# Kernel tuning notes

Measured on AMD Instinct MI355X. Metric: run time of the kernel, lower is better.

## Reference

```python
import jax, jax.numpy as jnp
import numpy as np

B, K, D = 4, 2048, 512   # batch, time window (self._K), d_model
H, Q, V = 8, 64, 64      # heads, per-head query dim, per-head value dim


def setup_inputs() -> dict:
    key = jax.random.key(0)
    ks = jax.random.split(key, 10)
    s = 0.05
    return {
        "query": jax.random.normal(ks[0], (B, K, D), jnp.float32),
        "key":   jax.random.normal(ks[1], (B, K, D), jnp.float32),
        "value": jax.random.normal(ks[2], (B, K, D), jnp.float32),
        # stacked per-head Linear params (torch Linear: y = x W^T + b -> store as [h, D, out])
        "W_q": jax.random.normal(ks[3], (H, D, Q), jnp.float32) * s,
        "b_q": jax.random.normal(ks[4], (H, Q), jnp.float32) * s,
        "W_k": jax.random.normal(ks[5], (H, D, Q), jnp.float32) * s,
        "b_k": jax.random.normal(ks[6], (H, Q), jnp.float32) * s,
        "W_v": jax.random.normal(ks[7], (H, D, V), jnp.float32) * s,
        "b_v": jax.random.normal(ks[8], (H, V), jnp.float32) * s,
        "W_o": jax.random.normal(ks[9], (H * V, D), jnp.float32) * s,
        "b_o": jnp.zeros((D,), jnp.float32),
    }


def reference(query, key, value, W_q, b_q, W_k, b_k, W_v, b_v, W_o, b_o):
    # per-head projections, batched over heads: [B, H, K, Q/V]
    q = jnp.einsum("bkd,hdq->bhkq", query, W_q) + b_q[None, :, None, :]
    k = jnp.einsum("bkd,hdq->bhkq", key,   W_k) + b_k[None, :, None, :]
    v = jnp.einsum("bkd,hdv->bhkv", value, W_v) + b_v[None, :, None, :]
    # NOTE: original divides by sqrt(self._K) (time window), NOT sqrt(d_k)
    scores = jnp.einsum("bhkq,bhlq->bhkl", q, k) / np.sqrt(K).astype(np.float32)
    # mask == 'subsequent': causal triu mask above the diagonal
    causal = jnp.triu(jnp.ones((K, K), bool), k=1)
    scores = jnp.where(causal[None, None], -jnp.inf, scores)
    attn = jax.nn.softmax(scores, axis=-1)
    heads = jnp.einsum("bhkl,bhlv->bhkv", attn, v)          # [B, H, K, V]
    concat = heads.transpose(0, 2, 1, 3).reshape(B, K, H * V)  # concat along last dim
    return concat @ W_o + b_o
```

## Files before the change

### kernel.cpp

```cpp
#include <hip/hip_runtime.h>
#include <hip/hip_bf16.h>

typedef __attribute__((ext_vector_type(8))) short bf16x8;
typedef __attribute__((ext_vector_type(4))) float f32x4;

#define SEQ 2048
#define DM  512
#define NH  8
#define DH  64
#define QSCALE 0.031879360f

__device__ __forceinline__ unsigned short f2bf(float f) {
  unsigned int u = __float_as_uint(f);
  unsigned int r = 0x7FFFu + ((u >> 16) & 1u);
  return (unsigned short)((u + r) >> 16);
}

__device__ __forceinline__ void cvt8f(const float4& v0, const float4& v1,
                                      unsigned short* __restrict__ o) {
  o[0] = f2bf(v0.x); o[1] = f2bf(v0.y); o[2] = f2bf(v0.z); o[3] = f2bf(v0.w);
  o[4] = f2bf(v1.x); o[5] = f2bf(v1.y); o[6] = f2bf(v1.z); o[7] = f2bf(v1.w);
}

__device__ __forceinline__ void load8f(const float* __restrict__ s,
                                       unsigned short* __restrict__ o) {
  float4 v0 = *(const float4*)s;
  float4 v1 = *(const float4*)(s + 4);
  cvt8f(v0, v1, o);
}

__global__ __launch_bounds__(256) void weight_prep(const float* __restrict__ Wq,
                                                   const float* __restrict__ Wk,
                                                   const float* __restrict__ Wv,
                                                   const float* __restrict__ Wo,
                                                   const float* __restrict__ q,
                                                   const float* __restrict__ k,
                                                   const float* __restrict__ v,
                                                   unsigned short* __restrict__ Wqt,
                                                   unsigned short* __restrict__ Wkt,
                                                   unsigned short* __restrict__ Wvt,
                                                   unsigned short* __restrict__ Wot,
                                                   unsigned short* __restrict__ Xb) {
  const int tid = threadIdx.x;
  if (blockIdx.x >= 256) {
    const int wi = blockIdx.x - 256;
    const float* src = (wi < 128) ? q : (wi < 256) ? k : v;
    const size_t off = (size_t)(wi & 127) * 32768;
    const float* s = src + off;
    unsigned short* d = Xb + (size_t)(wi >> 7) * (4u * SEQ * DM) + off;
#pragma unroll
    for (int i = 0; i < 16; ++i) {
      const size_t idx = (size_t)(tid + 256 * i) * 8;
      __align__(16) unsigned short t[8];
      load8f(s + idx, t);
      *(uint4*)(d + idx) = *(const uint4*)t;
    }
    return;
  }
  const int which = blockIdx.x >> 6, wi = blockIdx.x & 63;
  const float* src;
  unsigned short* dst;
  int R, C, r0, c0;
  if (which < 3) {
    const float* W = (which == 0) ? Wq : (which == 1) ? Wk : Wv;
    unsigned short* D = (which == 0) ? Wqt : (which == 1) ? Wkt : Wvt;
    int h = wi >> 3;
    src = W + (size_t)h * 512 * 64;
    dst = D + (size_t)h * 64 * 512;
    R = 512; C = 64; r0 = (wi & 7) * 64; c0 = 0;
  } else {
    src = Wo; dst = Wot;
    R = 512; C = 512; r0 = (wi >> 3) * 64; c0 = (wi & 7) * 64;
  }
  __shared__ __align__(16) unsigned short T[64][72];
#pragma unroll
  for (int i = 0; i < 2; ++i) {
    int c = tid + 256 * i;
    int lr = c >> 3, lc = (c & 7) * 8;
    __align__(16) unsigned short tmp[8];
    load8f(src + (size_t)(r0 + lr) * C + c0 + lc, tmp);
    *(uint4*)&T[lr][lc] = *(const uint4*)tmp;
  }
  __syncthreads();
#pragma unroll
  for (int i = 0; i < 2; ++i) {
    int c = tid + 256 * i;
    int orow = c >> 3, och = (c & 7) * 8;
    __align__(16) unsigned short tmp[8];
#pragma unroll
    for (int j = 0; j < 8; ++j) tmp[j] = T[och + j][orow];
    *(uint4*)(dst + (size_t)(c0 + orow) * R + r0 + och) = *(uint4*)tmp;
  }
}

__global__ __launch_bounds__(256, 4) void proj128(const unsigned short* __restrict__ Xb,
                                                  const unsigned short* __restrict__ Wqt,
                                                  const unsigned short* __restrict__ Wkt,
                                                  const unsigned short* __restrict__ Wvt,
                                                  const float* __restrict__ bq,
                                                  const float* __restrict__ bk,
                                                  const float* __restrict__ bv,
                                                  unsigned short* __restrict__ Qp,
                                                  unsigned short* __restrict__ Kp,
                                                  unsigned short* __restrict__ Vpt) {
  const int which = blockIdx.z;
  const unsigned short* X = Xb + (size_t)which * (4u * SEQ * DM);
  const unsigned short* Wt = (which == 0) ? Wqt : (which == 1) ? Wkt : Wvt;
  const float* bias = (which == 0) ? bq : (which == 1) ? bk : bv;
  unsigned short* out = (which == 0) ? Qp : (which == 1) ? Kp : Vpt;
  const float ps = (which == 0) ? QSCALE : 1.0f;

  const int m0 = blockIdx.x * 128;
  const int n0 = blockIdx.y * 128;
  __shared__ __align__(16) unsigned short smem[2][128][72];
  unsigned short (*As)[72] = smem[0];
  unsigned short (*Bs)[72] = smem[1];
  const int tid  = threadIdx.x;
  const int wave = tid >> 6, lane = tid & 63;
  const int l15  = lane & 15, quad = lane >> 4;
  const int rb = (wave >> 1) * 64, cb = (wave & 1) * 64;

  f32x4 acc[4][4];
#pragma unroll
  for (int i = 0; i < 4; ++i)
#pragma unroll
    for (int f = 0; f < 4; ++f) acc[i][f] = (f32x4){0.f, 0.f, 0.f, 0.f};

  for (int k0 = 0; k0 < DM; k0 += 64) {
    __syncthreads();
#pragma unroll
    for (int i = 0; i < 4; ++i) {
      int c = tid + 256 * i;
      int lr = c >> 3, lc = (c & 7) * 8;
      *(uint4*)&As[lr][lc] = *(const uint4*)(X  + (size_t)(m0 + lr) * DM + k0 + lc);
      *(uint4*)&Bs[lr][lc] = *(const uint4*)(Wt + (size_t)(n0 + lr) * DM + k0 + lc);
    }
    __syncthreads();
#pragma unroll
    for (int kc = 0; kc < 2; ++kc) {
      bf16x8 av[4], bv4[4];
#pragma unroll
      for (int i = 0; i < 4; ++i) av[i]  = *(const bf16x8*)&As[rb + 16 * i + l15][kc * 32 + quad * 8];
#pragma unroll
      for (int f = 0; f < 4; ++f) bv4[f] = *(const bf16x8*)&Bs[cb + 16 * f + l15][kc * 32 + quad * 8];
#pragma unroll
      for (int i = 0; i < 4; ++i)
#pragma unroll
        for (int f = 0; f < 4; ++f)
          acc[i][f] = __builtin_amdgcn_mfma_f32_16x16x32_bf16(av[i], bv4[f], acc[i][f], 0, 0, 0);
    }
  }

  if (which < 2) {
#pragma unroll
    for (int i = 0; i < 4; ++i)
#pragma unroll
      for (int f = 0; f < 4; ++f)
#pragma unroll
        for (int r = 0; r < 4; ++r) {
          int m = m0 + rb + 16 * i + quad * 4 + r;
          int col = n0 + cb + 16 * f + l15;
          int head = col >> 6, o = col & 63;
          int b = m >> 11, s = m & (SEQ - 1);
          float val = (acc[i][f][r] + bias[col]) * ps;
          out[(((size_t)(b * NH + head) * SEQ + s) << 6) + o] = f2bf(val);
        }
  } else {
    __syncthreads();
    unsigned short* T = &smem[0][0][0] + wave * 4608;
#pragma unroll
    for (int i = 0; i < 4; ++i)
#pragma unroll
      for (int f = 0; f < 4; ++f)
#pragma unroll
        for (int r = 0; r < 4; ++r) {
          int lrow = 16 * i + quad * 4 + r;
          int lcol = 16 * f + l15;
          int col = n0 + cb + 16 * f + l15;
          T[lcol * 72 + lrow] = f2bf(acc[i][f][r] + bias[col]);
        }
    const int mbase = m0 + rb;
    const int b = mbase >> 11, sbase = mbase & (SEQ - 1);
    const int head = (n0 + cb) >> 6;
    unsigned short* dstb = out + ((size_t)(b * NH + head) * DH) * SEQ + sbase;
#pragma unroll
    for (int j = 0; j < 8; ++j) {
      int dh = (lane >> 3) + j * 8;
      int sc = (lane & 7) * 8;
      *(uint4*)(dstb + (size_t)dh * SEQ + sc) = *(const uint4*)&T[dh * 72 + sc];
    }
  }
}

__global__ __launch_bounds__(512, 4) void attn_kernel(const unsigned short* __restrict__ Qp,
                                                      const unsigned short* __restrict__ Kp,
                                                      const unsigned short* __restrict__ Vpt,
                                                      unsigned short* __restrict__ concat) {
  const int bh = blockIdx.x;
  const int ip = blockIdx.y;
  const int b = bh >> 3, h = bh & 7;
  const int qa = ip, qb = 31 - ip;
  __shared__ __align__(16) unsigned short Ks[2][64][72], Vts[2][64][72], Ps[128][76];
  const int tid  = threadIdx.x;
  const int wave = tid >> 6, lane = tid & 63;
  const int l15  = lane & 15, quad = lane >> 4;
  const int w4   = wave & 3;
  const bool isB = wave < 4;
  const int qt   = isB ? qb : qa;
  const unsigned short* Qb = Qp  + (size_t)bh * SEQ * DH;
  const unsigned short* Kb = Kp  + (size_t)bh * SEQ * DH;
  const unsigned short* Vb = Vpt + (size_t)bh * DH * SEQ;

  bf16x8 aq[2];
#pragma unroll
  for (int kc = 0; kc < 2; ++kc)
    aq[kc] = *(const bf16x8*)(Qb + (size_t)(qt * 64 + 16 * w4 + l15) * DH + kc * 32 + quad * 8);

  float l_lane[4];
  f32x4 Of[4];
#pragma unroll
  for (int r = 0; r < 4; ++r) l_lane[r] = 0.f;
#pragma unroll
  for (int f = 0; f < 4; ++f) Of[f] = (f32x4){0.f, 0.f, 0.f, 0.f};

  const int sr = tid >> 3, sc = (tid & 7) * 8;
  uint4 kst, vst;

#define STAGE_LOAD(lt_) do {                                                   \
    kst = *(const uint4*)(Kb + (size_t)((lt_) * 64 + sr) * DH + sc);           \
    vst = *(const uint4*)(Vb + (size_t)sr * SEQ + (lt_) * 64 + sc);            \
  } while (0)

#define STAGE_WRITE(bi_) do {                                                  \
    *(uint4*)&Ks[bi_][sr][sc]  = kst;                                          \
    *(uint4*)&Vts[bi_][sr][sc] = vst;                                          \
  } while (0)

  STAGE_LOAD(0);
  STAGE_WRITE(0);
  STAGE_LOAD(1);
  __syncthreads();

#pragma unroll 1
  for (int lt = 0; lt <= qb; ++lt) {
    const int cur = lt & 1;
    if (lt < qb) STAGE_WRITE(cur ^ 1);
    if (lt + 2 <= qb) STAGE_LOAD(lt + 2);

    const bool act = isB || (lt <= qa);
    if (act) {
      const int l0 = lt * 64;
      f32x4 S[4];
#pragma unroll
      for (int f = 0; f < 4; ++f) S[f] = (f32x4){0.f, 0.f, 0.f, 0.f};
#pragma unroll
      for (int kc = 0; kc < 2; ++kc) {
#pragma unroll
        for (int f = 0; f < 4; ++f) {
          bf16x8 bk = *(const bf16x8*)&Ks[cur][16 * f + l15][kc * 32 + quad * 8];
          S[f] = __builtin_amdgcn_mfma_f32_16x16x32_bf16(aq[kc], bk, S[f], 0, 0, 0);
        }
      }
      if (lt == qt) {
        const int mrow = qt * 64 + 16 * w4 + quad * 4;
#pragma unroll
        for (int f = 0; f < 4; ++f)
#pragma unroll
          for (int r = 0; r < 4; ++r)
            if (l0 + 16 * f + l15 > mrow + r) S[f][r] = -1e30f;
      }
#pragma unroll
      for (int f = 0; f < 4; ++f)
#pragma unroll
        for (int r = 0; r < 4; ++r) {
          float p = __builtin_amdgcn_exp2f(S[f][r]);
          l_lane[r] += p;
          Ps[wave * 16 + quad * 4 + r][16 * f + l15] = f2bf(p);
        }
#pragma unroll
      for (int kc = 0; kc < 2; ++kc) {
        bf16x8 ap = *(const bf16x8*)&Ps[wave * 16 + l15][kc * 32 + quad * 8];
#pragma unroll
        for (int f = 0; f < 4; ++f) {
          bf16x8 bvv = *(const bf16x8*)&Vts[cur][16 * f + l15][kc * 32 + quad * 8];
          Of[f] = __builtin_amdgcn_mfma_f32_16x16x32_bf16(ap, bvv, Of[f], 0, 0, 0);
        }
      }
    }
    __syncthreads();
  }
#undef STAGE_LOAD
#undef STAGE_WRITE

#pragma unroll
  for (int d = 1; d < 16; d <<= 1)
#pragma unroll
    for (int r = 0; r < 4; ++r) l_lane[r] += __shfl_xor(l_lane[r], d);

#pragma unroll
  for (int f = 0; f < 4; ++f)
#pragma unroll
    for (int r = 0; r < 4; ++r) {
      const int row = qt * 64 + 16 * w4 + quad * 4 + r;
      const int col = h * DH + 16 * f + l15;
      concat[(size_t)(b * SEQ + row) * DM + col] = f2bf(Of[f][r] / l_lane[r]);
    }
}

__global__ __launch_bounds__(256, 2) void gemm_out(const unsigned short* __restrict__ A,
                                                   const unsigned short* __restrict__ Bt,
                                                   const float* __restrict__ bias,
                                                   float* __restrict__ out) {
  const int m0 = blockIdx.x * 64;
  const int nbase = blockIdx.y * 128;
  __shared__ __align__(16) unsigned short Bs[2][64][72];
  const int tid  = threadIdx.x;
  const int wave = tid >> 6, lane = tid & 63;
  const int l15  = lane & 15, quad = lane >> 4;

  bf16x8 afr[16];
  const unsigned short* arow = A + (size_t)(m0 + 16 * wave + l15) * DM;
#pragma unroll
  for (int k0i = 0; k0i < 8; ++k0i)
#pragma unroll
    for (int kc = 0; kc < 2; ++kc)
      afr[k0i * 2 + kc] = *(const bf16x8*)(arow + k0i * 64 + kc * 32 + quad * 8);

  uint4 bst0, bst1;
  const int br = tid >> 3, bc = (tid & 7) * 8;

#define G_LOAD(s_) do {                                                          \
    const int n0_ = nbase + ((s_) >> 3) * 64, k0_ = ((s_) & 7) * 64;             \
    bst0 = *(const uint4*)(Bt + (size_t)(n0_ + br) * DM + k0_ + bc);             \
    bst1 = *(const uint4*)(Bt + (size_t)(n0_ + br + 32) * DM + k0_ + bc);        \
  } while (0)

#define G_WRITE(bi_) do {                                                        \
    *(uint4*)&Bs[bi_][br][bc]      = bst0;                                       \
    *(uint4*)&Bs[bi_][br + 32][bc] = bst1;                                       \
  } while (0)

  f32x4 acc[2][4];
#pragma unroll
  for (int nh = 0; nh < 2; ++nh)
#pragma unroll
    for (int f = 0; f < 4; ++f) acc[nh][f] = (f32x4){0.f, 0.f, 0.f, 0.f};

  G_LOAD(0);
  G_WRITE(0);
  G_LOAD(1);
  __syncthreads();

#pragma unroll
  for (int s = 0; s < 16; ++s) {
    const int cur = s & 1;
    if (s < 15) G_WRITE(cur ^ 1);
    if (s < 14) G_LOAD(s + 2);
    const int nh = s >> 3, k0i = s & 7;
#pragma unroll
    for (int kc = 0; kc < 2; ++kc)
#pragma unroll
      for (int f = 0; f < 4; ++f) {
        bf16x8 bfv = *(const bf16x8*)&Bs[cur][16 * f + l15][kc * 32 + quad * 8];
        acc[nh][f] = __builtin_amdgcn_mfma_f32_16x16x32_bf16(afr[k0i * 2 + kc], bfv, acc[nh][f], 0, 0, 0);
      }
    __syncthreads();
  }
#undef G_LOAD
#undef G_WRITE

#pragma unroll
  for (int nh = 0; nh < 2; ++nh)
#pragma unroll
    for (int f = 0; f < 4; ++f)
#pragma unroll
      for (int r = 0; r < 4; ++r) {
        int row = 16 * wave + quad * 4 + r;
        int col = nbase + nh * 64 + 16 * f + l15;
        out[(size_t)(m0 + row) * DM + col] = acc[nh][f][r] + bias[col];
      }
}

extern "C" void kernel_launch(void* const* d_in, const int* in_sizes, int n_in,
                              void* d_out, int out_size, void* d_ws, size_t ws_size,
                              hipStream_t stream) {
  const float* query = (const float*)d_in[0];
  const float* key   = (const float*)d_in[1];
  const float* value = (const float*)d_in[2];
  const float* W_q   = (const float*)d_in[3];
  const float* b_q   = (const float*)d_in[4];
  const float* W_k   = (const float*)d_in[5];
  const float* b_k   = (const float*)d_in[6];
  const float* W_v   = (const float*)d_in[7];
  const float* b_v   = (const float*)d_in[8];
  const float* W_o   = (const float*)d_in[9];
  const float* b_o   = (const float*)d_in[10];
  float* out = (float*)d_out;

  char* ws = (char*)d_ws;
  unsigned short* Wqt    = (unsigned short*)(ws + 0);
  unsigned short* Wkt    = (unsigned short*)(ws + 524288);
  unsigned short* Wvt    = (unsigned short*)(ws + 1048576);
  unsigned short* Wot    = (unsigned short*)(ws + 1572864);
  unsigned short* Qp     = (unsigned short*)(ws + 2097152);
  unsigned short* Kp     = (unsigned short*)(ws + 10485760);
  unsigned short* Vpt    = (unsigned short*)(ws + 18874368);
  unsigned short* concat = (unsigned short*)(ws + 27262976);
  unsigned short* Xb     = (unsigned short*)(ws + 35651584);

  weight_prep<<<dim3(640), 256, 0, stream>>>(W_q, W_k, W_v, W_o, query, key, value,
                                             Wqt, Wkt, Wvt, Wot, Xb);

  proj128<<<dim3(64, 4, 3), 256, 0, stream>>>(Xb, Wqt, Wkt, Wvt,
                                              b_q, b_k, b_v, Qp, Kp, Vpt);

  attn_kernel<<<dim3(32, 16), 512, 0, stream>>>(Qp, Kp, Vpt, concat);

  gemm_out<<<dim3(128, 4), 256, 0, stream>>>(concat, Wot, b_o, out);
}
```

Measured before the change: 184.0 us.

## Keep softmax probabilities in registers via transposed QK MFMA and permlane swaps

Swaps the operands of the QK^T MFMA so each lane holds score columns for a single query row. The probabilities are then packed to bf16 with v_cvt_pk_bf16_f32 and rearranged into the PV A-operand layout with permlane32/16 swaps, so the shared-memory P buffer and its write/read round trip are gone. The row-sum reduction becomes a short cross-lane shuffle and the final division becomes a reciprocal multiply. The code relies on gfx950-specific instructions and on the lane mapping being exactly right, and smaller LDS use may allow higher occupancy.

New measurement: 176.8 us. 1.04x faster.

```diff
diff --git a/kernel.cpp b/kernel.cpp
--- a/kernel.cpp
+++ b/kernel.cpp
@@ -200,7 +200,7 @@
   const int ip = blockIdx.y;
   const int b = bh >> 3, h = bh & 7;
   const int qa = ip, qb = 31 - ip;
-  __shared__ __align__(16) unsigned short Ks[2][64][72], Vts[2][64][72], Ps[128][76];
+  __shared__ __align__(16) unsigned short Ks[2][64][72], Vts[2][64][72];
   const int tid  = threadIdx.x;
   const int wave = tid >> 6, lane = tid & 63;
   const int l15  = lane & 15, quad = lane >> 4;
@@ -216,10 +216,8 @@
   for (int kc = 0; kc < 2; ++kc)
     aq[kc] = *(const bf16x8*)(Qb + (size_t)(qt * 64 + 16 * w4 + l15) * DH + kc * 32 + quad * 8);
 
-  float l_lane[4];
+  float l_acc = 0.f;
   f32x4 Of[4];
-#pragma unroll
-  for (int r = 0; r < 4; ++r) l_lane[r] = 0.f;
 #pragma unroll
   for (int f = 0; f < 4; ++f) Of[f] = (f32x4){0.f, 0.f, 0.f, 0.f};
 
@@ -235,6 +233,10 @@
     *(uint4*)&Ks[bi_][sr][sc]  = kst;                                          \
     *(uint4*)&Vts[bi_][sr][sc] = vst;                                          \
   } while (0)
+
+#define CVTPK(d_, lo_, hi_) asm("v_cvt_pk_bf16_f32 %0, %1, %2" : "=v"(d_) : "v"(lo_), "v"(hi_))
+#define PL32SWAP(a_, b_) asm("v_permlane32_swap_b32 %0, %1" : "+v"(a_), "+v"(b_))
+#define PL16SWAP(a_, b_) asm("v_permlane16_swap_b32 %0, %1" : "+v"(a_), "+v"(b_))
 
   STAGE_LOAD(0);
   STAGE_WRITE(0);
@@ -249,7 +251,6 @@
 
     const bool act = isB || (lt <= qa);
     if (act) {
-      const int l0 = lt * 64;
       f32x4 S[4];
 #pragma unroll
       for (int f = 0; f < 4; ++f) S[f] = (f32x4){0.f, 0.f, 0.f, 0.f};
@@ -258,32 +259,40 @@
 #pragma unroll
         for (int f = 0; f < 4; ++f) {
           bf16x8 bk = *(const bf16x8*)&Ks[cur][16 * f + l15][kc * 32 + quad * 8];
-          S[f] = __builtin_amdgcn_mfma_f32_16x16x32_bf16(aq[kc], bk, S[f], 0, 0, 0);
+          S[f] = __builtin_amdgcn_mfma_f32_16x16x32_bf16(bk, aq[kc], S[f], 0, 0, 0);
         }
       }
       if (lt == qt) {
-        const int mrow = qt * 64 + 16 * w4 + quad * 4;
+        const int qloc = 16 * w4 + l15;
 #pragma unroll
         for (int f = 0; f < 4; ++f)
 #pragma unroll
           for (int r = 0; r < 4; ++r)
-            if (l0 + 16 * f + l15 > mrow + r) S[f][r] = -1e30f;
-      }
-#pragma unroll
-      for (int f = 0; f < 4; ++f)
-#pragma unroll
-        for (int r = 0; r < 4; ++r) {
-          float p = __builtin_amdgcn_exp2f(S[f][r]);
-          l_lane[r] += p;
-          Ps[wave * 16 + quad * 4 + r][16 * f + l15] = f2bf(p);
-        }
+            if (16 * f + 4 * quad + r > qloc) S[f][r] = -1e30f;
+      }
+      unsigned int P0[4], P1[4];
+#pragma unroll
+      for (int f = 0; f < 4; ++f) {
+        float p0 = __builtin_amdgcn_exp2f(S[f][0]);
+        float p1 = __builtin_amdgcn_exp2f(S[f][1]);
+        float p2 = __builtin_amdgcn_exp2f(S[f][2]);
+        float p3 = __builtin_amdgcn_exp2f(S[f][3]);
+        l_acc += (p0 + p1) + (p2 + p3);
+        CVTPK(P0[f], p0, p1);
+        CVTPK(P1[f], p2, p3);
+      }
 #pragma unroll
       for (int kc = 0; kc < 2; ++kc) {
-        bf16x8 ap = *(const bf16x8*)&Ps[wave * 16 + l15][kc * 32 + quad * 8];
+        unsigned int x0 = P0[2 * kc], y0 = P0[2 * kc + 1];
+        unsigned int x1 = P1[2 * kc], y1 = P1[2 * kc + 1];
+        PL32SWAP(x0, y0); PL16SWAP(x0, y0);
+        PL32SWAP(x1, y1); PL16SWAP(x1, y1);
+        union { unsigned int u[4]; bf16x8 v; } ap;
+        ap.u[0] = x0; ap.u[1] = x1; ap.u[2] = y0; ap.u[3] = y1;
 #pragma unroll
         for (int f = 0; f < 4; ++f) {
           bf16x8 bvv = *(const bf16x8*)&Vts[cur][16 * f + l15][kc * 32 + quad * 8];
-          Of[f] = __builtin_amdgcn_mfma_f32_16x16x32_bf16(ap, bvv, Of[f], 0, 0, 0);
+          Of[f] = __builtin_amdgcn_mfma_f32_16x16x32_bf16(ap.v, bvv, Of[f], 0, 0, 0);
         }
       }
     }
@@ -291,11 +300,15 @@
   }
 #undef STAGE_LOAD
 #undef STAGE_WRITE
-
-#pragma unroll
-  for (int d = 1; d < 16; d <<= 1)
-#pragma unroll
-    for (int r = 0; r < 4; ++r) l_lane[r] += __shfl_xor(l_lane[r], d);
+#undef CVTPK
+#undef PL32SWAP
+#undef PL16SWAP
+
+  l_acc += __shfl_xor(l_acc, 16);
+  l_acc += __shfl_xor(l_acc, 32);
+  float rl[4];
+#pragma unroll
+  for (int r = 0; r < 4; ++r) rl[r] = 1.0f / __shfl(l_acc, quad * 4 + r);
 
 #pragma unroll
   for (int f = 0; f < 4; ++f)
@@ -303,7 +316,7 @@
     for (int r = 0; r < 4; ++r) {
       const int row = qt * 64 + 16 * w4 + quad * 4 + r;
       const int col = h * DH + 16 * f + l15;
-      concat[(size_t)(b * SEQ + row) * DM + col] = f2bf(Of[f][r] / l_lane[r]);
+      concat[(size_t)(b * SEQ + row) * DM + col] = f2bf(Of[f][r] * rl[r]);
     }
 }
 
```
